# Kernel tuning notes

Measured on AMD Instinct MI355X. Metric: run time of the kernel, lower is better.

Reference implementation:

```python
import jax, jax.numpy as jnp
import numpy as np

B, IN, OUT, Q = 2048, 1024, 1024, 16

def setup_inputs() -> dict:
    key = jax.random.key(0)
    k1, k2, k3, k4 = jax.random.split(key, 4)
    bound = 1.0 / np.sqrt(IN)
    x = jax.random.normal(k1, (B, IN), dtype=jnp.float32)
    indices = jax.random.randint(k2, (B, IN), 0, Q, dtype=jnp.int32)
    # param_index: per-(quantile, input-feature) weight vector of length size_out
    param_table = jax.random.uniform(k3, (Q, IN, OUT), dtype=jnp.float32,
                                     minval=-bound, maxval=bound)
    bias = jax.random.uniform(k4, (OUT,), dtype=jnp.float32,
                              minval=-bound, maxval=bound)
    return {"x": x, "indices": indices, "param_table": param_table,
            "bias": bias, "store_activations": 0, "get_indices": 0, "use_db": 0}

def reference(x, indices, param_table, bias, store_activations, get_indices, use_db):
    # out[b, o] = sum_i param_table[indices[b,i], i, o] * x[b,i]  + bias[o]
    # Expressed as Q masked matmuls to avoid a [B, IN, OUT] gathered intermediate:
    # route each (b, i) contribution to its quantile's weight slab.
    q = param_table.shape[0]
    onehot = jax.nn.one_hot(indices, q, dtype=x.dtype)      # [B, IN, Q]
    xq = onehot * x[..., None]                               # [B, IN, Q]
    w_times_x = jnp.einsum('biq,qio->bo', xq, param_table)   # [B, OUT]
    return w_times_x + bias
```

## Files before the change

### kernel.cpp

```cpp
#include <hip/hip_runtime.h>
#include <stdint.h>

#define B_SZ   2048
#define IN_SZ  1024
#define OUT_SZ 1024
#define Q_SZ   16
#define NZB    4

typedef __attribute__((ext_vector_type(8))) short short8;
typedef __attribute__((ext_vector_type(4))) float floatx4;
typedef __attribute__((ext_vector_type(2))) unsigned short u16x2;
typedef __attribute__((ext_vector_type(2))) short s16x2;

__device__ __forceinline__ unsigned short f32_to_bf16_rne(float f) {
    union { float f; uint32_t u; } v; v.f = f;
    uint32_t u = v.u;
    return (unsigned short)((u + 0x7FFFu + ((u >> 16) & 1u)) >> 16);
}

__device__ __forceinline__ uint32_t mask3(uint32_t xv, uint32_t ohv, unsigned short sh) {
    union { uint32_t u; u16x2 v; s16x2 s; } t;
    t.u = ohv;
    u16x2 shv; shv.x = sh; shv.y = sh;
    t.v = t.v << shv;
    s16x2 f15; f15.x = 15; f15.y = 15;
    t.s = t.s >> f15;
    return xv & t.u;
}

__device__ __forceinline__ void gload_lds16(const void* g, void* l) {
    __builtin_amdgcn_global_load_lds(
        (const __attribute__((address_space(1))) unsigned int*)g,
        (__attribute__((address_space(3))) unsigned int*)l, 16, 0, 0);
}

__global__ void k_build_wf(const float* __restrict__ W, unsigned short* __restrict__ Wf) {
    const int S = blockIdx.x;
    const int q = S & 15, ih = (S >> 4) & 3, xb = (S >> 6) & 7, zb = S >> 9;
    const int t = threadIdx.x;
    const int i0 = zb * 256 + ih * 64;
    const int o0 = xb * 128;
    __shared__ unsigned short lds[64][130];

#pragma unroll
    for (int it = 0; it < 8; ++it) {
        int r  = it * 8 + (t >> 5);
        int c4 = (t & 31) * 4;
        float4 v = *(const float4*)(W + ((size_t)(q * 1024 + i0 + r)) * 1024 + o0 + c4);
        unsigned short h0 = f32_to_bf16_rne(v.x), h1 = f32_to_bf16_rne(v.y);
        unsigned short h2 = f32_to_bf16_rne(v.z), h3 = f32_to_bf16_rne(v.w);
        *(uint32_t*)&lds[r][c4]     = (uint32_t)h0 | ((uint32_t)h1 << 16);
        *(uint32_t*)&lds[r][c4 + 2] = (uint32_t)h2 | ((uint32_t)h3 << 16);
    }
    __syncthreads();

    unsigned short* dst = Wf + (size_t)S * 8192;
#pragma unroll
    for (int it = 0; it < 4; ++it) {
        int c = it * 256 + t;
        int L = c & 63;
        int hnt = c >> 6;
        int h = hnt >> 3, nt = hnt & 7;
        int ol = nt * 16 + (L & 15);
        int il = h * 32 + (L >> 4) * 8;
        unsigned short v[8];
#pragma unroll
        for (int j = 0; j < 8; ++j) v[j] = lds[il + j][ol];
        *(uint4*)(dst + (size_t)c * 8) = *(uint4*)v;
    }
}

__global__ __launch_bounds__(128, 1) void k_gemm(const unsigned short* __restrict__ Wf,
                                                 const float* __restrict__ x,
                                                 const int* __restrict__ idx,
                                                 float* __restrict__ P) {
    const int tid  = threadIdx.x;
    const int wave = tid >> 6, lane = tid & 63;

    const int id = blockIdx.x;
    const int zb = id & 3;
    const int xb = (id >> 2) & 7;
    const int yb = id >> 5;
    const int o0 = xb * 128, b0 = yb * 128, ibase = zb * 256;

    const char* wbase = (const char*)Wf + (size_t)(zb * 8 + xb) * 64 * 16384;
    const int   lofs  = lane * 16;

    __shared__ unsigned char sm[4][16384];

    const int arow = b0 + wave * 64 + (lane & 15);
    const float* xg = x + (size_t)arow * IN_SZ + ibase + (lane >> 4) * 8;
    const int*   ig = idx + (size_t)arow * IN_SZ + ibase + (lane >> 4) * 8;

    floatx4 acc[32];
#pragma unroll
    for (int i = 0; i < 32; ++i) acc[i] = (floatx4){0.f, 0.f, 0.f, 0.f};

    uint4 xr[4][2], oh[4][2];
    short8 fc[8], fn[8];

#define RELOADA(ih)                                                           \
    {   int io_ = (ih) * 64;                                                  \
        _Pragma("unroll")                                                     \
        for (int mt_ = 0; mt_ < 4; ++mt_)                                     \
            _Pragma("unroll")                                                 \
            for (int hh_ = 0; hh_ < 2; ++hh_) {                               \
                const float* xp_ = xg + mt_ * 16 * IN_SZ + io_ + hh_ * 32;    \
                const int*   ip_ = ig + mt_ * 16 * IN_SZ + io_ + hh_ * 32;    \
                float a_[8]; int b_[8];                                       \
                *(float4*)(a_)     = *(const float4*)xp_;                     \
                *(float4*)(a_ + 4) = *((const float4*)xp_ + 1);               \
                *(int4*)(b_)       = *(const int4*)ip_;                       \
                *(int4*)(b_ + 4)   = *((const int4*)ip_ + 1);                 \
                unsigned short xv_[8];                                        \
                _Pragma("unroll")                                             \
                for (int j_ = 0; j_ < 8; ++j_) xv_[j_] = f32_to_bf16_rne(a_[j_]); \
                xr[mt_][hh_] = *(uint4*)xv_;                                  \
                uint32_t iw_[4];                                              \
                _Pragma("unroll")                                             \
                for (int w_ = 0; w_ < 4; ++w_)                                \
                    iw_[w_] = (1u << b_[2 * w_]) | ((1u << b_[2 * w_ + 1]) << 16); \
                oh[mt_][hh_] = *(uint4*)iw_;                                  \
            }                                                                 \
    }

#define MASKS(hh)                                                             \
        _Pragma("unroll")                                                     \
        for (int mt_ = 0; mt_ < 4; ++mt_) {                                   \
            aF[mt_].u.x = mask3(xr[mt_][hh].x, oh[mt_][hh].x, sh_);           \
            aF[mt_].u.y = mask3(xr[mt_][hh].y, oh[mt_][hh].y, sh_);           \
            aF[mt_].u.z = mask3(xr[mt_][hh].z, oh[mt_][hh].z, sh_);           \
            aF[mt_].u.w = mask3(xr[mt_][hh].w, oh[mt_][hh].w, sh_);           \
        }

    const int soff = wave * 8192 + lofs;
#define STAGE(s_, r_)                                                         \
    {   const char* gp_ = wbase + (size_t)(s_) * 16384 + soff;                \
        unsigned char* lp_ = (unsigned char*)sm + (r_) * 16384 + soff;        \
        _Pragma("unroll")                                                     \
        for (int u_ = 0; u_ < 8; ++u_)                                        \
            gload_lds16(gp_ + u_ * 1024, lp_ + u_ * 1024);                    \
    }

#define DSREAD(dst, rr, hofs)                                                 \
    {   const unsigned char* bp_ = (const unsigned char*)sm + (rr) * 16384 +  \
                                   (hofs) + lofs;                             \
        _Pragma("unroll")                                                     \
        for (int nt_ = 0; nt_ < 8; ++nt_)                                     \
            (dst)[nt_] = *(const short8*)(bp_ + nt_ * 1024);                  \
    }

#define MFMA32(fa)                                                            \
        _Pragma("unroll")                                                     \
        for (int mt_ = 0; mt_ < 4; ++mt_)                                     \
            _Pragma("unroll")                                                 \
            for (int nt_ = 0; nt_ < 8; ++nt_)                                 \
                acc[mt_ * 8 + nt_] = __builtin_amdgcn_mfma_f32_16x16x32_bf16( \
                    aF[mt_].s8, (fa)[nt_], acc[mt_ * 8 + nt_], 0, 0, 0);

#define SLAB(s_, rc_, rn_, rs_)                                               \
    {   if ((s_) < 62) STAGE((s_) + 2, rs_);                                  \
        DSREAD(fn, rc_, 8192);                                                \
        const unsigned short sh_ = (unsigned short)(15 - ((s_) & 15));        \
        union { uint4 u; short8 s8; } aF[4];                                  \
        MASKS(0);                                                             \
        MFMA32(fc);                                                           \
        if ((s_) < 63) DSREAD(fc, rn_, 0);                                    \
        MASKS(1);                                                             \
        MFMA32(fn);                                                           \
        __syncthreads();                                                      \
    }

    RELOADA(0);
    STAGE(0, 0);
    STAGE(1, 1);
    __syncthreads();
    DSREAD(fc, 0, 0);

#pragma unroll 1
    for (int gg = 0; gg < 16; ++gg) {
        if (gg && (gg & 3) == 0) RELOADA(gg >> 2);
        const int s0 = gg * 4;
        SLAB(s0 + 0, 0, 1, 2);
        SLAB(s0 + 1, 1, 2, 3);
        SLAB(s0 + 2, 2, 3, 0);
        SLAB(s0 + 3, 3, 0, 1);
    }

    float* Pz = P + (size_t)zb * (B_SZ * OUT_SZ);
    int cn = lane & 15, rq = lane >> 4;
#pragma unroll
    for (int mt = 0; mt < 4; ++mt)
#pragma unroll
        for (int nt = 0; nt < 8; ++nt) {
            int bb = b0 + wave * 64 + mt * 16 + rq * 4;
            int oo = o0 + nt * 16 + cn;
#pragma unroll
            for (int e = 0; e < 4; ++e)
                Pz[(size_t)(bb + e) * OUT_SZ + oo] = acc[mt * 8 + nt][e];
        }
#undef RELOADA
#undef MASKS
#undef STAGE
#undef DSREAD
#undef MFMA32
#undef SLAB
}

__global__ void k_reduce(const float* __restrict__ P, const float* __restrict__ bias,
                         float* __restrict__ out) {
    int t = blockIdx.x * 256 + threadIdx.x;
    const float4* b4 = (const float4*)bias;
    float4 a = b4[t & 255];
#pragma unroll
    for (int z = 0; z < NZB; ++z) {
        float4 v = ((const float4*)P)[(size_t)z * (B_SZ * OUT_SZ / 4) + t];
        a.x += v.x; a.y += v.y; a.z += v.z; a.w += v.w;
    }
    ((float4*)out)[t] = a;
}

__global__ void k_naive(const float* __restrict__ x, const int* __restrict__ idx,
                        const float* __restrict__ W, const float* __restrict__ bias,
                        float* __restrict__ out) {
    int b = blockIdx.x;
    int o = threadIdx.x * 4;
    float4 acc = *(const float4*)(bias + o);
    const float* xr = x + (size_t)b * IN_SZ;
    const int*   ir = idx + (size_t)b * IN_SZ;
    for (int i = 0; i < IN_SZ; ++i) {
        float xv = xr[i];
        int q = ir[i];
        float4 w4 = *(const float4*)(W + ((size_t)q * IN_SZ + i) * OUT_SZ + o);
        acc.x += xv * w4.x; acc.y += xv * w4.y;
        acc.z += xv * w4.z; acc.w += xv * w4.w;
    }
    *(float4*)(out + (size_t)b * OUT_SZ + o) = acc;
}

extern "C" void kernel_launch(void* const* d_in, const int* in_sizes, int n_in,
                              void* d_out, int out_size, void* d_ws, size_t ws_size,
                              hipStream_t stream) {
    const float* x    = (const float*)d_in[0];
    const int*   idx  = (const int*)d_in[1];
    const float* W    = (const float*)d_in[2];
    const float* bias = (const float*)d_in[3];
    float* out = (float*)d_out;

    const size_t wf_bytes = (size_t)2048 * 16384;
    const size_t p_bytes  = (size_t)NZB * B_SZ * OUT_SZ * 4;
    if (ws_size < wf_bytes + p_bytes) {
        k_naive<<<dim3(B_SZ), dim3(256), 0, stream>>>(x, idx, W, bias, out);
        return;
    }
    unsigned short* Wf = (unsigned short*)d_ws;
    float* P = (float*)((char*)d_ws + wf_bytes);

    k_build_wf<<<dim3(2048), dim3(256), 0, stream>>>(W, Wf);
    k_gemm<<<dim3(NZB * 8 * (B_SZ / 128)), dim3(128), 0, stream>>>(Wf, x, idx, P);
    k_reduce<<<dim3(2048), dim3(256), 0, stream>>>(P, bias, out);
}
```

Baseline: 203.1 us.

## Retile GEMM to 256x64 blocks with four waves and two blocks per CU

```diff
diff --git a/kernel.cpp b/kernel.cpp
--- a/kernel.cpp
+++ b/kernel.cpp
@@ -70,7 +70,7 @@
     }
 }
 
-__global__ __launch_bounds__(128, 1) void k_gemm(const unsigned short* __restrict__ Wf,
+__global__ __launch_bounds__(256, 2) void k_gemm(const unsigned short* __restrict__ Wf,
                                                  const float* __restrict__ x,
                                                  const int* __restrict__ idx,
                                                  float* __restrict__ P) {
@@ -79,25 +79,26 @@
 
     const int id = blockIdx.x;
     const int zb = id & 3;
-    const int xb = (id >> 2) & 7;
-    const int yb = id >> 5;
-    const int o0 = xb * 128, b0 = yb * 128, ibase = zb * 256;
-
-    const char* wbase = (const char*)Wf + (size_t)(zb * 8 + xb) * 64 * 16384;
+    const int xb = (id >> 2) & 15;
+    const int yb = id >> 6;
+    const int xbW = xb >> 1, xh = xb & 1;
+    const int o0 = xb * 64, b0 = yb * 256, ibase = zb * 256;
+
+    const char* wbase = (const char*)Wf + (size_t)(zb * 8 + xbW) * 64 * 16384
+                        + (size_t)xh * 4096;
     const int   lofs  = lane * 16;
 
-    __shared__ unsigned char sm[4][16384];
+    __shared__ unsigned char sm[4][8192];
 
     const int arow = b0 + wave * 64 + (lane & 15);
     const float* xg = x + (size_t)arow * IN_SZ + ibase + (lane >> 4) * 8;
     const int*   ig = idx + (size_t)arow * IN_SZ + ibase + (lane >> 4) * 8;
 
-    floatx4 acc[32];
-#pragma unroll
-    for (int i = 0; i < 32; ++i) acc[i] = (floatx4){0.f, 0.f, 0.f, 0.f};
+    floatx4 acc[16];
+#pragma unroll
+    for (int i = 0; i < 16; ++i) acc[i] = (floatx4){0.f, 0.f, 0.f, 0.f};
 
     uint4 xr[4][2], oh[4][2];
-    short8 fc[8], fn[8];
 
 #define RELOADA(ih)                                                           \
     {   int io_ = (ih) * 64;                                                  \
@@ -133,58 +134,59 @@
             aF[mt_].u.w = mask3(xr[mt_][hh].w, oh[mt_][hh].w, sh_);           \
         }
 
-    const int soff = wave * 8192 + lofs;
+    const int hsel = (wave >> 1), qsel = (wave & 1);
+    const int sofs = hsel * 8192 + qsel * 2048 + lofs;
+    const int dofs = hsel * 4096 + qsel * 2048 + lofs;
 #define STAGE(s_, r_)                                                         \
-    {   const char* gp_ = wbase + (size_t)(s_) * 16384 + soff;                \
-        unsigned char* lp_ = (unsigned char*)sm + (r_) * 16384 + soff;        \
-        _Pragma("unroll")                                                     \
-        for (int u_ = 0; u_ < 8; ++u_)                                        \
-            gload_lds16(gp_ + u_ * 1024, lp_ + u_ * 1024);                    \
-    }
-
-#define DSREAD(dst, rr, hofs)                                                 \
-    {   const unsigned char* bp_ = (const unsigned char*)sm + (rr) * 16384 +  \
-                                   (hofs) + lofs;                             \
-        _Pragma("unroll")                                                     \
-        for (int nt_ = 0; nt_ < 8; ++nt_)                                     \
-            (dst)[nt_] = *(const short8*)(bp_ + nt_ * 1024);                  \
-    }
-
-#define MFMA32(fa)                                                            \
+    {   const char* gp_ = wbase + (size_t)(s_) * 16384 + sofs;                \
+        unsigned char* lp_ = (unsigned char*)sm + (r_) * 8192 + dofs;         \
+        gload_lds16(gp_,        lp_);                                         \
+        gload_lds16(gp_ + 1024, lp_ + 1024);                                  \
+    }
+
+#define SLABC(s_, r_)                                                         \
+    {   const unsigned short sh_ = (unsigned short)(15 - ((s_) & 15));        \
+        union { uint4 u; short8 s8; } aF[4];                                  \
+        short8 f0[4], f1[4];                                                  \
+        const unsigned char* bp_ = (const unsigned char*)sm + (r_) * 8192 + lofs; \
+        _Pragma("unroll")                                                     \
+        for (int nt_ = 0; nt_ < 4; ++nt_)                                     \
+            f0[nt_] = *(const short8*)(bp_ + nt_ * 1024);                     \
+        _Pragma("unroll")                                                     \
+        for (int nt_ = 0; nt_ < 4; ++nt_)                                     \
+            f1[nt_] = *(const short8*)(bp_ + 4096 + nt_ * 1024);              \
+        MASKS(0);                                                             \
         _Pragma("unroll")                                                     \
         for (int mt_ = 0; mt_ < 4; ++mt_)                                     \
             _Pragma("unroll")                                                 \
-            for (int nt_ = 0; nt_ < 8; ++nt_)                                 \
-                acc[mt_ * 8 + nt_] = __builtin_amdgcn_mfma_f32_16x16x32_bf16( \
-                    aF[mt_].s8, (fa)[nt_], acc[mt_ * 8 + nt_], 0, 0, 0);
-
-#define SLAB(s_, rc_, rn_, rs_)                                               \
-    {   if ((s_) < 62) STAGE((s_) + 2, rs_);                                  \
-        DSREAD(fn, rc_, 8192);                                                \
-        const unsigned short sh_ = (unsigned short)(15 - ((s_) & 15));        \
-        union { uint4 u; short8 s8; } aF[4];                                  \
-        MASKS(0);                                                             \
-        MFMA32(fc);                                                           \
-        if ((s_) < 63) DSREAD(fc, rn_, 0);                                    \
+            for (int nt_ = 0; nt_ < 4; ++nt_)                                 \
+                acc[mt_ * 4 + nt_] = __builtin_amdgcn_mfma_f32_16x16x32_bf16( \
+                    aF[mt_].s8, f0[nt_], acc[mt_ * 4 + nt_], 0, 0, 0);        \
         MASKS(1);                                                             \
-        MFMA32(fn);                                                           \
-        __syncthreads();                                                      \
+        _Pragma("unroll")                                                     \
+        for (int mt_ = 0; mt_ < 4; ++mt_)                                     \
+            _Pragma("unroll")                                                 \
+            for (int nt_ = 0; nt_ < 4; ++nt_)                                 \
+                acc[mt_ * 4 + nt_] = __builtin_amdgcn_mfma_f32_16x16x32_bf16( \
+                    aF[mt_].s8, f1[nt_], acc[mt_ * 4 + nt_], 0, 0, 0);        \
     }
 
     RELOADA(0);
     STAGE(0, 0);
     STAGE(1, 1);
     __syncthreads();
-    DSREAD(fc, 0, 0);
 
 #pragma unroll 1
-    for (int gg = 0; gg < 16; ++gg) {
-        if (gg && (gg & 3) == 0) RELOADA(gg >> 2);
-        const int s0 = gg * 4;
-        SLAB(s0 + 0, 0, 1, 2);
-        SLAB(s0 + 1, 1, 2, 3);
-        SLAB(s0 + 2, 2, 3, 0);
-        SLAB(s0 + 3, 3, 0, 1);
+    for (int gg = 0; gg < 32; ++gg) {
+        if (gg && (gg & 7) == 0) RELOADA(gg >> 3);
+        const int s0 = 2 * gg;
+        if (gg < 31) {
+            STAGE(s0 + 2, (s0 + 2) & 3);
+            STAGE(s0 + 3, (s0 + 3) & 3);
+        }
+        SLABC(s0,     s0 & 3);
+        SLABC(s0 + 1, (s0 + 1) & 3);
+        __syncthreads();
     }
 
     float* Pz = P + (size_t)zb * (B_SZ * OUT_SZ);
@@ -192,19 +194,17 @@
 #pragma unroll
     for (int mt = 0; mt < 4; ++mt)
 #pragma unroll
-        for (int nt = 0; nt < 8; ++nt) {
+        for (int nt = 0; nt < 4; ++nt) {
             int bb = b0 + wave * 64 + mt * 16 + rq * 4;
             int oo = o0 + nt * 16 + cn;
 #pragma unroll
             for (int e = 0; e < 4; ++e)
-                Pz[(size_t)(bb + e) * OUT_SZ + oo] = acc[mt * 8 + nt][e];
+                Pz[(size_t)(bb + e) * OUT_SZ + oo] = acc[mt * 4 + nt][e];
         }
 #undef RELOADA
 #undef MASKS
 #undef STAGE
-#undef DSREAD
-#undef MFMA32
-#undef SLAB
+#undef SLABC
 }
 
 __global__ void k_reduce(const float* __restrict__ P, const float* __restrict__ bias,
@@ -257,6 +257,6 @@
     float* P = (float*)((char*)d_ws + wf_bytes);
 
     k_build_wf<<<dim3(2048), dim3(256), 0, stream>>>(W, Wf);
-    k_gemm<<<dim3(NZB * 8 * (B_SZ / 128)), dim3(128), 0, stream>>>(Wf, x, idx, P);
+    k_gemm<<<dim3(4 * 16 * (B_SZ / 256)), dim3(256), 0, stream>>>(Wf, x, idx, P);
     k_reduce<<<dim3(2048), dim3(256), 0, stream>>>(P, bias, out);
 }
```

Result: no change. 203.1 us (-0.0%).
